# Kernel tuning notes

Measured on AMD Instinct MI355X. Metric: run time of the kernel, lower is better.

## Reference

```python
import jax, jax.numpy as jnp
import numpy as np

N_NODES = 100000
N_EDGES = 3200000
D_IN = 256
D_OUT = 256


def setup_inputs() -> dict:
    key = jax.random.key(0)
    k1, k2, k3, k4, k5 = jax.random.split(key, 5)
    x = jax.random.normal(k1, (N_NODES, D_IN), dtype=jnp.float32)
    weight = jax.random.normal(k2, (D_IN, D_OUT), dtype=jnp.float32)
    edge_rows = jax.random.randint(k3, (N_EDGES,), 0, N_NODES, dtype=jnp.int32)
    edge_cols = jax.random.randint(k4, (N_EDGES,), 0, N_NODES, dtype=jnp.int32)
    edge_vals = jax.random.uniform(k5, (N_EDGES,), dtype=jnp.float32)
    return {"x": x, "weight": weight, "edge_rows": edge_rows,
            "edge_cols": edge_cols, "edge_vals": edge_vals}


def reference(x, weight, edge_rows, edge_cols, edge_vals):
    # GraphConvolution forward (eval mode, dense features, no bias):
    #   xw  = x @ W                      [N, D_OUT]
    #   out = relu(A_sparse @ xw)        A given as COO edge list
    xw = x @ weight  # [N, D_OUT]
    msgs = edge_vals[:, None] * xw[edge_cols]  # gather source features, scale
    agg = jax.ops.segment_sum(msgs, edge_rows, num_segments=N_NODES)
    return jax.nn.relu(agg)
```

## Files before the change

### kernel.cpp

```cpp
#include <hip/hip_runtime.h>
#include <hip/hip_bf16.h>

#define N_NODES 100000
#define N_EDGES 3200000
#define D 256

#define RSH3 6
#define RPB3 64
#define NB3 ((N_NODES + RPB3 - 1) / RPB3)
#define FILL_CH 14336
#define NBLK_F ((N_EDGES + FILL_CH - 1) / FILL_CH)
#define BCAP 2560
#define OCAP 64

typedef __attribute__((ext_vector_type(8))) short short8;
typedef __attribute__((ext_vector_type(4))) float floatx4;

__device__ __forceinline__ unsigned short f32_to_bf16_rne(float f) {
    unsigned int u = __float_as_uint(f);
    u += 0x7FFFu + ((u >> 16) & 1u);
    return (unsigned short)(u >> 16);
}
__device__ __forceinline__ float bf16_bits_to_f32(unsigned short b) {
    return __uint_as_float(((unsigned int)b) << 16);
}
__device__ __forceinline__ float blo(unsigned int x) { return __uint_as_float(x << 16); }
__device__ __forceinline__ float bhi(unsigned int x) { return __uint_as_float(x & 0xFFFF0000u); }

__global__ __launch_bounds__(256) void convert_w_k(const float* __restrict__ w,
                                                   unsigned short* __restrict__ wsw) {
    int t = blockIdx.x * 256 + threadIdx.x;
    int j     = t & 7;
    int lane  = (t >> 3) & 63;
    int kstep = (t >> 9) & 7;
    int ntile = t >> 12;
    int k = kstep * 32 + (lane >> 4) * 8 + j;
    int n = ntile * 16 + (lane & 15);
    wsw[t] = f32_to_bf16_rne(w[k * D + n]);
}

__global__ __launch_bounds__(512) void gemm_xw_k(const float* __restrict__ x,
                                                 const unsigned short* __restrict__ wsw,
                                                 unsigned short* __restrict__ xwb) {
    __shared__ uint4 wlds[8192];
    const int tid = threadIdx.x;
#pragma unroll
    for (int i = 0; i < 16; ++i) {
        int idx = i * 512 + tid;
        wlds[idx] = ((const uint4*)wsw)[idx];
    }
    __syncthreads();

    const int lane = tid & 63;
    const int wave = tid >> 6;
    const int q    = lane >> 4;
    const int ml   = lane & 15;
    const long rowBase = (long)blockIdx.x * 128 + wave * 16;
    long arow = rowBase + ml;
    if (arow >= N_NODES) arow = 0;
    const float* xr = x + arow * (long)D;

    floatx4 acc[16];
#pragma unroll
    for (int i = 0; i < 16; ++i) acc[i] = (floatx4){0.f, 0.f, 0.f, 0.f};

    const short8* wfrag = (const short8*)wlds;

#pragma unroll
    for (int ks = 0; ks < 8; ++ks) {
        const float4 a0 = *(const float4*)(xr + ks * 32 + q * 8);
        const float4 a1 = *(const float4*)(xr + ks * 32 + q * 8 + 4);
        short8 af;
        af[0] = (short)f32_to_bf16_rne(a0.x);
        af[1] = (short)f32_to_bf16_rne(a0.y);
        af[2] = (short)f32_to_bf16_rne(a0.z);
        af[3] = (short)f32_to_bf16_rne(a0.w);
        af[4] = (short)f32_to_bf16_rne(a1.x);
        af[5] = (short)f32_to_bf16_rne(a1.y);
        af[6] = (short)f32_to_bf16_rne(a1.z);
        af[7] = (short)f32_to_bf16_rne(a1.w);
#pragma unroll
        for (int nt = 0; nt < 16; ++nt) {
            acc[nt] = __builtin_amdgcn_mfma_f32_16x16x32_bf16(
                af, wfrag[(nt * 8 + ks) * 64 + lane], acc[nt], 0, 0, 0);
        }
    }

#pragma unroll
    for (int nt = 0; nt < 16; ++nt) {
#pragma unroll
        for (int r = 0; r < 4; ++r) {
            long orow = rowBase + q * 4 + r;
            if (orow < N_NODES)
                xwb[orow * (long)D + nt * 16 + ml] = f32_to_bf16_rne(acc[nt][r]);
        }
    }
}

__global__ __launch_bounds__(256) void hist2_k(const int* __restrict__ erow,
                                               int* __restrict__ C) {
    __shared__ int h[NB3];
    const int tid = threadIdx.x;
    for (int i = tid; i < NB3; i += 256) h[i] = 0;
    __syncthreads();
    const int s = blockIdx.x * FILL_CH;
    const int e = min(s + FILL_CH, N_EDGES);
    for (int i = s + tid; i < e; i += 256) atomicAdd(&h[erow[i] >> RSH3], 1);
    __syncthreads();
    for (int b = tid; b < NB3; b += 256) C[b * NBLK_F + blockIdx.x] = h[b];
}

__global__ __launch_bounds__(256) void colprefix_k(int* __restrict__ C,
                                                   int* __restrict__ tot) {
    const int wave_id = blockIdx.x * 4 + (threadIdx.x >> 6);
    const int lane = threadIdx.x & 63;
    if (wave_id >= NB3) return;
    int* row = C + wave_id * NBLK_F;
    int run = 0;
#pragma unroll
    for (int ch = 0; ch < NBLK_F; ch += 64) {
        int idx = ch + lane;
        int v = (idx < NBLK_F) ? row[idx] : 0;
        int x = v;
#pragma unroll
        for (int d = 1; d < 64; d <<= 1) {
            int u = __shfl_up(x, d);
            if (lane >= d) x += u;
        }
        int excl = x - v;
        if (idx < NBLK_F) row[idx] = run + excl;
        run += __shfl(x, 63);
    }
    if (lane == 0) tot[wave_id] = run;
}

__global__ __launch_bounds__(1024) void totscan_k(const int* __restrict__ tot,
                                                  int* __restrict__ bbase) {
    __shared__ int wsum[16];
    const int t = threadIdx.x;
    const int lane = t & 63;
    const int wv = t >> 6;
    const int b0 = 2 * t, b1 = 2 * t + 1;
    int v0 = (b0 < NB3) ? tot[b0] : 0;
    int v1 = (b1 < NB3) ? tot[b1] : 0;
    int sv = v0 + v1;
    int x = sv;
#pragma unroll
    for (int d = 1; d < 64; d <<= 1) {
        int u = __shfl_up(x, d);
        if (lane >= d) x += u;
    }
    if (lane == 63) wsum[wv] = x;
    __syncthreads();
    if (wv == 0) {
        int y = (lane < 16) ? wsum[lane] : 0;
#pragma unroll
        for (int d = 1; d < 16; d <<= 1) {
            int u = __shfl_up(y, d);
            if (lane >= d) y += u;
        }
        if (lane < 16) wsum[lane] = y;
    }
    __syncthreads();
    int excl = x - sv + ((wv > 0) ? wsum[wv - 1] : 0);
    if (b0 < NB3) bbase[b0] = excl;
    if (b1 < NB3) bbase[b1] = excl + v0;
    if (b0 == NB3 - 1) bbase[NB3] = excl + v0;
    if (b1 == NB3 - 1) bbase[NB3] = excl + v0 + v1;
}

__global__ __launch_bounds__(512) void binfill3_k(const int* __restrict__ erow,
                                                  const int* __restrict__ ecol,
                                                  const float* __restrict__ eval,
                                                  const int* __restrict__ C,
                                                  const int* __restrict__ bbase,
                                                  unsigned long long* __restrict__ recs) {
    __shared__ unsigned long long lrec[FILL_CH];
    __shared__ int h[NB3];
    __shared__ int cur[NB3];
    __shared__ int gb[NB3];
    __shared__ int wsum[8];
    const int tid = threadIdx.x;
    const int blk = blockIdx.x;
    const int s = blk * FILL_CH;
    const int e = min(s + FILL_CH, N_EDGES);

    for (int i = tid; i < NB3; i += 512) h[i] = 0;
    __syncthreads();

    for (int i = s + tid; i < e; i += 512) atomicAdd(&h[erow[i] >> RSH3], 1);
    __syncthreads();

    {
        const int b0 = 4 * tid;
        int v0 = (b0     < NB3) ? h[b0]     : 0;
        int v1 = (b0 + 1 < NB3) ? h[b0 + 1] : 0;
        int v2 = (b0 + 2 < NB3) ? h[b0 + 2] : 0;
        int v3 = (b0 + 3 < NB3) ? h[b0 + 3] : 0;
        int s4 = v0 + v1 + v2 + v3;
        const int lane = tid & 63;
        const int wv = tid >> 6;
        int x = s4;
#pragma unroll
        for (int d = 1; d < 64; d <<= 1) {
            int u = __shfl_up(x, d);
            if (lane >= d) x += u;
        }
        if (lane == 63) wsum[wv] = x;
        __syncthreads();
        if (wv == 0) {
            int y = (lane < 8) ? wsum[lane] : 0;
#pragma unroll
            for (int d = 1; d < 8; d <<= 1) {
                int u = __shfl_up(y, d);
                if (lane >= d) y += u;
            }
            if (lane < 8) wsum[lane] = y;
        }
        __syncthreads();
        int excl = x - s4 + ((wv > 0) ? wsum[wv - 1] : 0);
        if (b0     < NB3) cur[b0]     = excl;
        if (b0 + 1 < NB3) cur[b0 + 1] = excl + v0;
        if (b0 + 2 < NB3) cur[b0 + 2] = excl + v0 + v1;
        if (b0 + 3 < NB3) cur[b0 + 3] = excl + v0 + v1 + v2;
    }
    for (int b = tid; b < NB3; b += 512) gb[b] = bbase[b] + C[b * NBLK_F + blk];
    __syncthreads();

    for (int i = s + tid; i < e; i += 512) {
        int r = erow[i];
        int b = r >> RSH3;
        unsigned long long rec =
            ((unsigned long long)(r & (RPB3 - 1)) << 33) |
            ((unsigned long long)f32_to_bf16_rne(eval[i]) << 17) |
            (unsigned int)ecol[i];
        int pos = atomicAdd(&cur[b], 1);
        lrec[pos] = rec;
    }
    __syncthreads();

    const int lane = tid & 63;
    const int wv = tid >> 6;
    for (int b = wv; b < NB3; b += 8) {
        int len = h[b];
        int start = cur[b] - len;
        int gdst = gb[b];
        for (int o = lane; o < len; o += 64) recs[gdst + o] = lrec[start + o];
    }
}

__global__ __launch_bounds__(256) void baggr_k(const unsigned short* __restrict__ xwb,
                                               const int* __restrict__ bbase,
                                               const unsigned long long* __restrict__ recs,
                                               float* __restrict__ out) {
    __shared__ unsigned long long lrec[BCAP];
    __shared__ unsigned long long ovfl[OCAP];
    __shared__ int hist[RPB3];
    __shared__ int cur[RPB3];
    __shared__ int novf;
    const int t = threadIdx.x;
    const int b = blockIdx.x;
    const int base = bbase[b];
    const int nfull = bbase[b + 1] - base;

    if (t < RPB3) hist[t] = 0;
    if (t == 0) novf = 0;
    __syncthreads();
    for (int i = t; i < nfull; i += 256)
        atomicAdd(&hist[(int)((recs[base + i] >> 33) & 63u)], 1);
    __syncthreads();

    if (t < 64) {
        int v = hist[t];
        int x = v;
#pragma unroll
        for (int d = 1; d < 64; d <<= 1) {
            int u = __shfl_up(x, d);
            if (t >= d) x += u;
        }
        cur[t] = x - v;
    }
    __syncthreads();

    for (int i = t; i < nfull; i += 256) {
        unsigned long long rec = recs[base + i];
        int rl = (int)((rec >> 33) & 63u);
        int pos = atomicAdd(&cur[rl], 1);
        if (pos < BCAP) lrec[pos] = rec;
        else {
            int o = atomicAdd(&novf, 1);
            if (o < OCAP) ovfl[o] = rec;
        }
    }
    __syncthreads();

    const int wave = t >> 6;
    const int lane = t & 63;
    const int half = lane >> 5;
    const int hl   = lane & 31;
    const int nov  = min(novf, OCAP);

#pragma unroll 1
    for (int rr = 0; rr < 16; ++rr) {
        const int rl = wave * 16 + rr;
        const int r = (b << RSH3) + rl;
        if (r >= N_NODES) break;
        const int e_ = cur[rl];
        const int s_ = e_ - hist[rl];
        const int e = min(e_, BCAP);
        const int s = min(s_, BCAP);

        float acc[8];
#pragma unroll
        for (int k = 0; k < 8; ++k) acc[k] = 0.f;

#pragma unroll 1
        for (int jb = s; jb < e; jb += 64) {
            const int cnt = min(64, e - jb);
            const int pairs = (cnt + 1) >> 1;
            const int hp = cnt >> 1;
            int tt = 0;

#define FMA8(qv, bv)                                                           \
            acc[0] += bv * blo(qv.x); acc[1] += bv * bhi(qv.x);                \
            acc[2] += bv * blo(qv.y); acc[3] += bv * bhi(qv.y);                \
            acc[4] += bv * blo(qv.z); acc[5] += bv * bhi(qv.z);                \
            acc[6] += bv * blo(qv.w); acc[7] += bv * bhi(qv.w);
#define SLOTL(ss, qv, bv)                                                      \
            {                                                                  \
                int src = jb + 2 * (tt + (ss)) + half;                         \
                unsigned long long rec = lrec[src];                            \
                unsigned int bc = (unsigned int)(rec & 0x1FFFFu);              \
                bv = bf16_bits_to_f32((unsigned short)((rec >> 17) & 0xFFFFu));\
                qv = ((const uint4*)(xwb + (size_t)bc * D))[hl];               \
            }

#pragma unroll 1
            for (; tt + 8 <= hp; tt += 8) {
                uint4 q0, q1, q2, q3, q4, q5, q6, q7;
                float b0, b1, b2, b3, b4, b5, b6, b7;
                SLOTL(0, q0, b0) SLOTL(1, q1, b1) SLOTL(2, q2, b2) SLOTL(3, q3, b3)
                SLOTL(4, q4, b4) SLOTL(5, q5, b5) SLOTL(6, q6, b6) SLOTL(7, q7, b7)
                FMA8(q0, b0) FMA8(q1, b1) FMA8(q2, b2) FMA8(q3, b3)
                FMA8(q4, b4) FMA8(q5, b5) FMA8(q6, b6) FMA8(q7, b7)
            }
            if (tt + 4 <= hp) {
                uint4 q0, q1, q2, q3;
                float b0, b1, b2, b3;
                SLOTL(0, q0, b0) SLOTL(1, q1, b1) SLOTL(2, q2, b2) SLOTL(3, q3, b3)
                FMA8(q0, b0) FMA8(q1, b1) FMA8(q2, b2) FMA8(q3, b3)
                tt += 4;
            }
#undef SLOTL
#pragma unroll 1
            for (; tt < pairs; ++tt) {
                int src = jb + 2 * tt + half;
                int srcc = min(src, e - 1);
                unsigned long long rec = lrec[srcc];
                unsigned int bc = (unsigned int)(rec & 0x1FFFFu);
                float vv = bf16_bits_to_f32((unsigned short)((rec >> 17) & 0xFFFFu));
                float bv = (src < e) ? vv : 0.f;
                uint4 q = ((const uint4*)(xwb + (size_t)bc * D))[hl];
                FMA8(q, bv)
            }
        }

#pragma unroll 1
        for (int k = 0; k < nov; ++k) {
            unsigned long long rec = ovfl[k];
            if ((int)((rec >> 33) & 63u) == rl) {
                unsigned int bc = (unsigned int)(rec & 0x1FFFFu);
                float vv = bf16_bits_to_f32((unsigned short)((rec >> 17) & 0xFFFFu));
                float bv = (half == 0) ? vv : 0.f;
                uint4 q = ((const uint4*)(xwb + (size_t)bc * D))[hl];
                FMA8(q, bv)
            }
        }
#undef FMA8

#pragma unroll
        for (int k = 0; k < 8; ++k) acc[k] += __shfl_xor(acc[k], 32);

        const int sl = lane >> 1;
        const int par = lane & 1;
        float4 o;
        {
            float a0 = __shfl(acc[0], sl), c0 = __shfl(acc[4], sl);
            float a1 = __shfl(acc[1], sl), c1 = __shfl(acc[5], sl);
            float a2 = __shfl(acc[2], sl), c2 = __shfl(acc[6], sl);
            float a3 = __shfl(acc[3], sl), c3 = __shfl(acc[7], sl);
            o.x = par ? c0 : a0;
            o.y = par ? c1 : a1;
            o.z = par ? c2 : a2;
            o.w = par ? c3 : a3;
        }
        o.x = fmaxf(o.x, 0.f);
        o.y = fmaxf(o.y, 0.f);
        o.z = fmaxf(o.z, 0.f);
        o.w = fmaxf(o.w, 0.f);
        ((float4*)(out + (size_t)r * D))[lane] = o;
    }
}

extern "C" void kernel_launch(void* const* d_in, const int* in_sizes, int n_in,
                              void* d_out, int out_size, void* d_ws, size_t ws_size,
                              hipStream_t stream) {
    const float* x    = (const float*)d_in[0];
    const float* w    = (const float*)d_in[1];
    const int*   erow = (const int*)d_in[2];
    const int*   ecol = (const int*)d_in[3];
    const float* eval = (const float*)d_in[4];
    float* out = (float*)d_out;

    char* p = (char*)d_ws;
    auto align = [](size_t v) { return (v + 255) & ~(size_t)255; };

    unsigned short* xwb = (unsigned short*)p;
    p += align((size_t)N_NODES * D * sizeof(unsigned short));
    unsigned short* wsw = (unsigned short*)p;
    p += align((size_t)D * D * sizeof(unsigned short));
    int* C     = (int*)p;  p += align((size_t)NB3 * NBLK_F * sizeof(int));
    int* tot   = (int*)p;  p += align((size_t)NB3 * sizeof(int));
    int* bbase = (int*)p;  p += align((size_t)(NB3 + 1) * sizeof(int));
    unsigned long long* recs = (unsigned long long*)p;
    p += align((size_t)N_EDGES * sizeof(unsigned long long));

    convert_w_k<<<(D * D) / 256, 256, 0, stream>>>(w, wsw);
    gemm_xw_k<<<(N_NODES + 127) / 128, 512, 0, stream>>>(x, wsw, xwb);
    hist2_k<<<NBLK_F, 256, 0, stream>>>(erow, C);
    colprefix_k<<<(NB3 + 3) / 4, 256, 0, stream>>>(C, tot);
    totscan_k<<<1, 1024, 0, stream>>>(tot, bbase);
    binfill3_k<<<NBLK_F, 512, 0, stream>>>(erow, ecol, eval, C, bbase, recs);
    baggr_k<<<NB3, 256, 0, stream>>>(xwb, bbase, recs, out);
}
```

Before: 545.8 us.

## Stage GEMM output through swizzled LDS; register-cache records and split LDS record arrays

The GEMM epilogue now writes bf16 results into LDS with an XOR swizzle and then stores full rows with 16-byte vector writes, replacing scattered 2-byte global stores. The aggregation kernel reads each block's records once into registers, reusing them for both the histogram and scatter passes instead of loading from global memory twice. It also stores the records in LDS as separate column and value arrays, which makes room for a larger per-block capacity (3072 instead of 2560) and reduces overflow. The register array raises register pressure and may lower occupancy.

```diff
diff --git a/kernel.cpp b/kernel.cpp
--- a/kernel.cpp
+++ b/kernel.cpp
@@ -10,7 +10,8 @@
 #define NB3 ((N_NODES + RPB3 - 1) / RPB3)
 #define FILL_CH 14336
 #define NBLK_F ((N_EDGES + FILL_CH - 1) / FILL_CH)
-#define BCAP 2560
+#define RCAP 12
+#define SCAP 3072
 #define OCAP 64
 
 typedef __attribute__((ext_vector_type(8))) short short8;
@@ -55,8 +56,8 @@
     const int wave = tid >> 6;
     const int q    = lane >> 4;
     const int ml   = lane & 15;
-    const long rowBase = (long)blockIdx.x * 128 + wave * 16;
-    long arow = rowBase + ml;
+    const long rowBase = (long)blockIdx.x * 128;
+    long arow = rowBase + wave * 16 + ml;
     if (arow >= N_NODES) arow = 0;
     const float* xr = x + arow * (long)D;
 
@@ -86,13 +87,29 @@
         }
     }
 
+    __syncthreads();
+    unsigned short* lds16 = (unsigned short*)wlds;
 #pragma unroll
     for (int nt = 0; nt < 16; ++nt) {
 #pragma unroll
         for (int r = 0; r < 4; ++r) {
-            long orow = rowBase + q * 4 + r;
-            if (orow < N_NODES)
-                xwb[orow * (long)D + nt * 16 + ml] = f32_to_bf16_rne(acc[nt][r]);
+            int rowL = wave * 16 + q * 4 + r;
+            int chunk = (nt * 2 + (ml >> 3)) ^ (rowL & 7);
+            lds16[rowL * 256 + chunk * 8 + (ml & 7)] = f32_to_bf16_rne(acc[nt][r]);
+        }
+    }
+    __syncthreads();
+    {
+        int rowL = tid >> 2;
+        long gRow = rowBase + rowL;
+        if (gRow < N_NODES) {
+            const uint4* src = (const uint4*)(lds16 + rowL * 256);
+            uint4* dst = (uint4*)(xwb + gRow * (long)D);
+#pragma unroll
+            for (int c8 = 0; c8 < 8; ++c8) {
+                int chunk = (tid & 3) * 8 + c8;
+                dst[chunk] = src[chunk ^ (rowL & 7)];
+            }
         }
     }
 }
@@ -253,7 +270,8 @@
                                                const int* __restrict__ bbase,
                                                const unsigned long long* __restrict__ recs,
                                                float* __restrict__ out) {
-    __shared__ unsigned long long lrec[BCAP];
+    __shared__ unsigned int   cols[SCAP];
+    __shared__ unsigned short vals[SCAP];
     __shared__ unsigned long long ovfl[OCAP];
     __shared__ int hist[RPB3];
     __shared__ int cur[RPB3];
@@ -261,13 +279,25 @@
     const int t = threadIdx.x;
     const int b = blockIdx.x;
     const int base = bbase[b];
-    const int nfull = bbase[b + 1] - base;
+    const int bend = bbase[b + 1];
 
     if (t < RPB3) hist[t] = 0;
     if (t == 0) novf = 0;
     __syncthreads();
-    for (int i = t; i < nfull; i += 256)
-        atomicAdd(&hist[(int)((recs[base + i] >> 33) & 63u)], 1);
+
+    unsigned long long myrec[RCAP];
+#pragma unroll
+    for (int k = 0; k < RCAP; ++k) {
+        int idx = base + k * 256 + t;
+        if (idx < bend) myrec[k] = recs[idx];
+    }
+#pragma unroll
+    for (int k = 0; k < RCAP; ++k) {
+        int idx = base + k * 256 + t;
+        if (idx < bend) atomicAdd(&hist[(int)((myrec[k] >> 33) & 63u)], 1);
+    }
+    for (int i = base + RCAP * 256 + t; i < bend; i += 256)
+        atomicAdd(&hist[(int)((recs[i] >> 33) & 63u)], 1);
     __syncthreads();
 
     if (t < 64) {
@@ -282,12 +312,30 @@
     }
     __syncthreads();
 
-    for (int i = t; i < nfull; i += 256) {
-        unsigned long long rec = recs[base + i];
+#pragma unroll
+    for (int k = 0; k < RCAP; ++k) {
+        int idx = base + k * 256 + t;
+        if (idx < bend) {
+            unsigned long long rec = myrec[k];
+            int rl = (int)((rec >> 33) & 63u);
+            int pos = atomicAdd(&cur[rl], 1);
+            if (pos < SCAP) {
+                cols[pos] = (unsigned int)(rec & 0x1FFFFu);
+                vals[pos] = (unsigned short)((rec >> 17) & 0xFFFFu);
+            } else {
+                int o = atomicAdd(&novf, 1);
+                if (o < OCAP) ovfl[o] = rec;
+            }
+        }
+    }
+    for (int i = base + RCAP * 256 + t; i < bend; i += 256) {
+        unsigned long long rec = recs[i];
         int rl = (int)((rec >> 33) & 63u);
         int pos = atomicAdd(&cur[rl], 1);
-        if (pos < BCAP) lrec[pos] = rec;
-        else {
+        if (pos < SCAP) {
+            cols[pos] = (unsigned int)(rec & 0x1FFFFu);
+            vals[pos] = (unsigned short)((rec >> 17) & 0xFFFFu);
+        } else {
             int o = atomicAdd(&novf, 1);
             if (o < OCAP) ovfl[o] = rec;
         }
@@ -307,8 +355,8 @@
         if (r >= N_NODES) break;
         const int e_ = cur[rl];
         const int s_ = e_ - hist[rl];
-        const int e = min(e_, BCAP);
-        const int s = min(s_, BCAP);
+        const int e = min(e_, SCAP);
+        const int s = min(s_, SCAP);
 
         float acc[8];
 #pragma unroll
@@ -329,9 +377,8 @@
 #define SLOTL(ss, qv, bv)                                                      \
             {                                                                  \
                 int src = jb + 2 * (tt + (ss)) + half;                         \
-                unsigned long long rec = lrec[src];                            \
-                unsigned int bc = (unsigned int)(rec & 0x1FFFFu);              \
-                bv = bf16_bits_to_f32((unsigned short)((rec >> 17) & 0xFFFFu));\
+                unsigned int bc = cols[src];                                   \
+                bv = bf16_bits_to_f32(vals[src]);                              \
                 qv = ((const uint4*)(xwb + (size_t)bc * D))[hl];               \
             }
 
@@ -356,9 +403,8 @@
             for (; tt < pairs; ++tt) {
                 int src = jb + 2 * tt + half;
                 int srcc = min(src, e - 1);
-                unsigned long long rec = lrec[srcc];
-                unsigned int bc = (unsigned int)(rec & 0x1FFFFu);
-                float vv = bf16_bits_to_f32((unsigned short)((rec >> 17) & 0xFFFFu));
+                unsigned int bc = cols[srcc];
+                float vv = bf16_bits_to_f32(vals[srcc]);
                 float bv = (src < e) ? vv : 0.f;
                 uint4 q = ((const uint4*)(xwb + (size_t)bc * D))[hl];
                 FMA8(q, bv)
```

Result: no change. 554.6 us (+1.6%).
